# Optimization experiments

Hardware: AMD Instinct MI355X
Metric: run time of the kernel (lower is better)

The kernel has to match this reference:

```python
import jax, jax.numpy as jnp
import numpy as np

NUM_USERS = 100000
NUM_ITEMS = 50000
NUM_HIDDEN = 64
NUM_BINS = 10
BATCH = 131072
N_QUAD = 64  # quadrature nodes in incomplete/complete beta
EPS = 1e-6


def _trapz0(y, dt):
    # trapezoidal rule along axis 0 with uniform spacing dt
    return (jnp.sum(y, axis=0) - 0.5 * (y[0] + y[-1])) * dt


def setup_inputs() -> dict:
    key = jax.random.key(0)
    ks = jax.random.split(key, 12)
    return {
        "uid_input": jax.random.randint(ks[0], (BATCH,), 0, NUM_USERS),
        "iid_input": jax.random.randint(ks[1], (BATCH,), 0, NUM_ITEMS),
        "uid_features": 0.1 * jax.random.normal(ks[2], (NUM_USERS, NUM_HIDDEN + 1), jnp.float32),
        "iid_features": 0.1 * jax.random.normal(ks[3], (NUM_ITEMS, NUM_HIDDEN + 1), jnp.float32),
        "uid_bin_terms": 0.1 * jax.random.normal(ks[4], (NUM_USERS, NUM_BINS), jnp.float32),
        "iid_bin_terms": 0.1 * jax.random.normal(ks[5], (NUM_ITEMS, NUM_BINS), jnp.float32),
        "uid_alpha_emb": 0.01 * jax.random.normal(ks[6], (NUM_USERS, 1), jnp.float32),
        "uid_beta_emb": 0.01 * jax.random.normal(ks[7], (NUM_USERS, 1), jnp.float32),
        "iid_alpha_emb": 0.01 * jax.random.normal(ks[8], (NUM_ITEMS, 1), jnp.float32),
        "iid_beta_emb": 0.01 * jax.random.normal(ks[9], (NUM_ITEMS, 1), jnp.float32),
        "global_bias": jnp.asarray(2.0, jnp.float32),
    }


def reference(uid_input, iid_input, uid_features, iid_features,
              uid_bin_terms, iid_bin_terms, uid_alpha_emb, uid_beta_emb,
              iid_alpha_emb, iid_beta_emb, global_bias):
    # embedding lookups (confidence features alias the regular features)
    uf = uid_features[uid_input]          # (B, H+1)
    vf = iid_features[iid_input]          # (B, H+1)
    u = uf[:, :-1]                        # (B, H)
    v = vf[:, :-1]

    # mu / upsilon (upsilon_layer_id == 2: |dot|)
    dot = jnp.sum(u * v, axis=-1, keepdims=True)                    # (B, 1)
    len_prod = (jnp.linalg.norm(u, axis=1, keepdims=True)
                * jnp.linalg.norm(v, axis=1, keepdims=True))
    mu = jnp.clip(0.5 + 0.5 * dot / jnp.maximum(len_prod, EPS), EPS, 1.0 - EPS)
    upsilon = jnp.maximum(jnp.abs(dot), EPS)

    # alpha / beta
    alpha = jnp.maximum(0.01, mu * upsilon)
    beta = jnp.maximum(0.01, upsilon - alpha)
    alpha = global_bias + alpha
    beta = global_bias + beta
    alpha = jnp.maximum(0.01, alpha + uid_alpha_emb[uid_input] + iid_alpha_emb[iid_input])  # (B,1)
    beta = jnp.maximum(0.01, beta + uid_beta_emb[uid_input] + iid_beta_emb[iid_input])      # (B,1)

    # per-pair bin edges via normalized exp + cumsum
    terms = jnp.exp(uid_bin_terms[uid_input] + iid_bin_terms[iid_input])  # (B, NUM_BINS)
    terms = terms / jnp.sum(terms, axis=-1, keepdims=True)
    edges = jnp.cumsum(terms, axis=-1)                                    # (B, NUM_BINS)

    # regularized incomplete beta at interior edges via trapezoidal quadrature
    x = edges[:, :-1]                                  # (B, NB-1)
    t = jnp.linspace(0.0, 1.0, N_QUAD, dtype=alpha.dtype)
    dt = t[1] - t[0]
    t3 = t[:, None, None]                              # (n, 1, 1)
    a3 = alpha[None, :, :]                             # (1, B, 1)
    b3 = beta[None, :, :]
    tx = t3 * x[None]                                  # (n, B, NB-1)
    integrand = (tx ** (a3 - 1.0)) * ((1.0 - tx) ** (b3 - 1.0))
    integrand = integrand * (t3 <= x[None]).astype(integrand.dtype)
    Bx_ab = _trapz0(integrand, dt)                     # (B, NB-1)

    # complete beta B(a, b)
    c_int = (t[None, :] ** (alpha - 1.0)) * ((1.0 - t[None, :]) ** (beta - 1.0))  # (B, n)
    B_ab = (jnp.sum(c_int, axis=-1) - 0.5 * (c_int[:, 0] + c_int[:, -1])) * dt    # (B,)

    cdf = Bx_ab / B_ab[:, None]                        # (B, NB-1)
    cdf = jnp.concatenate([cdf, jnp.ones_like(alpha)], axis=-1)  # (B, NB)
    mass = jnp.concatenate([cdf[:, :1], cdf[:, 1:] - cdf[:, :-1]], axis=-1)
    return mass
```

## Files before the change

kernel.cpp:

```cpp
#include <hip/hip_runtime.h>
#include <math.h>

#define BLOCK 256

struct F4a4 { float a, b, c, d; };

__device__ __forceinline__ float exp2_fast(float x) {
#if __has_builtin(__builtin_amdgcn_exp2f)
    return __builtin_amdgcn_exp2f(x);
#else
    return __expf(x * 0.69314718055994531f);
#endif
}

__device__ __forceinline__ double exp_f64_fast(double x) {
    const double L2E = 1.4426950408889634074;
    const double LN2 = 0.69314718055994530942;
    double z = x * L2E;
    double n = rint(z);
    double r = fma(x, L2E, -n);
    double w = r * LN2;
    double p = 2.08767569878680989792e-9;
    p = fma(p, w, 2.50521083854417187751e-8);
    p = fma(p, w, 2.75573192239858906526e-7);
    p = fma(p, w, 2.75573192239858925110e-6);
    p = fma(p, w, 2.48015873015873015873e-5);
    p = fma(p, w, 1.98412698412698412698e-4);
    p = fma(p, w, 1.38888888888888888889e-3);
    p = fma(p, w, 8.33333333333333333333e-3);
    p = fma(p, w, 4.16666666666666666667e-2);
    p = fma(p, w, 1.66666666666666666667e-1);
    p = fma(p, w, 0.5);
    p = fma(p, w, 1.0);
    p = fma(p, w, 1.0);
    const int ni = (int)n;
    const double sc = __longlong_as_double((long long)(1023 + ni) << 52);
    return p * sc;
}

__global__ __launch_bounds__(BLOCK) void lbd_kernel(
    const int* __restrict__ uid_in, const int* __restrict__ iid_in,
    const float* __restrict__ uf,  const float* __restrict__ vf,
    const float* __restrict__ ubt, const float* __restrict__ ibt,
    const float* __restrict__ uae, const float* __restrict__ ube,
    const float* __restrict__ iae, const float* __restrict__ ibe,
    const float* __restrict__ gbp, float* __restrict__ out, int B)
{
    const int tid = threadIdx.x;
    const int sub = tid & 15;
    const int s0  = blockIdx.x * (BLOCK / 16) + (tid >> 4);
    const bool valid = (s0 < B);
    const int s = valid ? s0 : (B - 1);

    const int u = uid_in[s];
    const int v = iid_in[s];

    const F4a4 a = ((const F4a4*)(uf + (long long)u * 65))[sub];
    const F4a4 b = ((const F4a4*)(vf + (long long)v * 65))[sub];

    float dotp = a.a * b.a + a.b * b.b + a.c * b.c + a.d * b.d;
    float sup  = a.a * a.a + a.b * a.b + a.c * a.c + a.d * a.d;
    float svp  = b.a * b.a + b.b * b.b + b.c * b.c + b.d * b.d;
#pragma unroll
    for (int d = 1; d < 16; d <<= 1) {
        dotp += __shfl_xor(dotp, d, 64);
        sup  += __shfl_xor(sup,  d, 64);
        svp  += __shfl_xor(svp,  d, 64);
    }

    const float gb = gbp[0];
    const float len_prod = sqrtf(sup) * sqrtf(svp);
    const float EPS = 1e-6f;
    const float HI  = (float)(1.0 - 1e-6);
    float mu = 0.5f + (0.5f * dotp) / fmaxf(len_prod, EPS);
    mu = fminf(fmaxf(mu, EPS), HI);
    const float ups = fmaxf(fabsf(dotp), EPS);
    const float al0 = fmaxf(0.01f, mu * ups);
    const float be0 = fmaxf(0.01f, ups - al0);
    const float alpha = fmaxf(0.01f, (gb + al0) + uae[u] + iae[v]);
    const float beta  = fmaxf(0.01f, (gb + be0) + ube[u] + ibe[v]);
    const float am1 = alpha - 1.0f;
    const float bm1 = beta  - 1.0f;

    const double STEP = 1.0 / 63.0;
    float xf_own = 0.f, lx_own = 0.f;
    int   im_own = 0;
    {
        double e = 0.0;
        if (sub < 10)
            e = exp_f64_fast((double)ubt[u * 10 + sub] + (double)ibt[v * 10 + sub]);
        double c = e;
#pragma unroll
        for (int d = 1; d < 16; d <<= 1) {
            double t = __shfl_up(c, d, 16);
            if (sub >= d) c += t;
        }
        const double ssum = __shfl(c, 9, 16);
        if (sub < 9) {
            const double x = c / ssum;
            int k = (int)(x * 63.0);
            k = (k > 62) ? 62 : k;
            const int dec = ((double)k * STEP > x) ? 1 : 0;
            const int inc = ((k < 62) && ((double)(k + 1) * STEP <= x)) ? 1 : 0;
            im_own = k + inc - dec;
            xf_own = (float)x;
            lx_own = __log2f(xf_own);
        }
    }
    float xfj[9], alxj[9];
    int   imj[9];
#pragma unroll
    for (int j = 0; j < 9; ++j) {
        xfj[j]  = __shfl(xf_own, j, 16);
        alxj[j] = am1 * __shfl(lx_own, j, 16);
        imj[j]  = __shfl(im_own, j, 16);
    }

    float tfm[4], altm[4], l1m[4];
#pragma unroll
    for (int m = 0; m < 4; ++m) {
        const int i = m * 16 + sub;
        const float tf = (float)((double)i * STEP);
        tfm[m]  = tf;
        altm[m] = am1 * __log2f(tf);
        l1m[m]  = __log2f(1.0f - tf);
    }

    float accD = 0.0f;
    float acc[9];
#pragma unroll
    for (int j = 0; j < 9; ++j) acc[j] = 0.0f;

#pragma unroll
    for (int m = 0; m < 4; ++m)
        accD += exp2_fast(fmaf(bm1, l1m[m], altm[m]));

#pragma unroll
    for (int m = 0; m < 4; ++m) {
#pragma unroll
        for (int j = 0; j < 9; ++j) {
            const float w_ = fmaf(-tfm[m], xfj[j], 1.0f);
            const float e_ = fmaf(bm1, __log2f(w_), altm[m] + alxj[j]);
            const float y_ = exp2_fast(e_);
            const int   i_ = m * 16 + sub;
            acc[j] += ((unsigned)(i_ - 1) < (unsigned)imj[j]) ? y_ : 0.0f;
        }
    }

#pragma unroll
    for (int d = 1; d < 16; d <<= 1) {
        accD += __shfl_xor(accD, d, 64);
#pragma unroll
        for (int j = 0; j < 9; ++j) acc[j] += __shfl_xor(acc[j], d, 64);
    }

    const float dtf = (float)(1.0 / 63.0);
    const float Bab = accD * dtf;
    const float rB  = 1.0f / Bab;
    float cdfv[9];
#pragma unroll
    for (int j = 0; j < 9; ++j) cdfv[j] = (acc[j] * dtf) * rB;

    float mo = cdfv[0];
#pragma unroll
    for (int j = 1; j < 9; ++j) mo = (sub == j) ? (cdfv[j] - cdfv[j - 1]) : mo;
    mo = (sub == 9) ? (1.0f - cdfv[8]) : mo;
    if (valid && sub < 10) out[(long long)s * 10 + sub] = mo;
}

extern "C" void kernel_launch(void* const* d_in, const int* in_sizes, int n_in,
                              void* d_out, int out_size, void* d_ws, size_t ws_size,
                              hipStream_t stream) {
    (void)n_in; (void)out_size; (void)d_ws; (void)ws_size;
    const int*   uid = (const int*)d_in[0];
    const int*   iid = (const int*)d_in[1];
    const float* uf  = (const float*)d_in[2];
    const float* vf  = (const float*)d_in[3];
    const float* ubt = (const float*)d_in[4];
    const float* ibt = (const float*)d_in[5];
    const float* uae = (const float*)d_in[6];
    const float* ube = (const float*)d_in[7];
    const float* iae = (const float*)d_in[8];
    const float* ibe = (const float*)d_in[9];
    const float* gb  = (const float*)d_in[10];
    float* out = (float*)d_out;
    const int B = in_sizes[0];
    const int samples_per_block = BLOCK / 16;
    const int grid = (B + samples_per_block - 1) / samples_per_block;
    hipLaunchKernelGGL(lbd_kernel, dim3(grid), dim3(BLOCK), 0, stream,
                       uid, iid, uf, vf, ubt, ibt, uae, ube, iae, ibe, gb, out, B);
}
```

Baseline: 133.0 us.

## Use 4 lanes per sample with LDS node tables and wave-uniform early loop exit

Each sample now gets 4 lanes instead of 16, so every lane covers 16 quadrature nodes and 3 bin edges. The quadrature node values and their logs are precomputed once per block into shared memory. The per-edge integration loop now stops at a wave-uniform bound taken from the max edge index across the wave, which skips nodes past each edge that the mask would zero anyway. This reduces redundant log/exp work and the shuffle reduction depth, at the cost of more per-lane serial work, a __syncthreads, and a data-dependent loop trip count that may limit unrolling.

```diff
diff --git a/kernel.cpp b/kernel.cpp
--- a/kernel.cpp
+++ b/kernel.cpp
@@ -2,6 +2,7 @@
 #include <math.h>
 
 #define BLOCK 256
+#define SPB (BLOCK / 4)
 
 struct F4a4 { float a, b, c, d; };
 
@@ -16,8 +17,7 @@
 __device__ __forceinline__ double exp_f64_fast(double x) {
     const double L2E = 1.4426950408889634074;
     const double LN2 = 0.69314718055994530942;
-    double z = x * L2E;
-    double n = rint(z);
+    double n = rint(x * L2E);
     double r = fma(x, L2E, -n);
     double w = r * LN2;
     double p = 2.08767569878680989792e-9;
@@ -33,8 +33,7 @@
     p = fma(p, w, 0.5);
     p = fma(p, w, 1.0);
     p = fma(p, w, 1.0);
-    const int ni = (int)n;
-    const double sc = __longlong_as_double((long long)(1023 + ni) << 52);
+    const double sc = __longlong_as_double((long long)(1023 + (int)n) << 52);
     return p * sc;
 }
 
@@ -46,23 +45,41 @@
     const float* __restrict__ iae, const float* __restrict__ ibe,
     const float* __restrict__ gbp, float* __restrict__ out, int B)
 {
+    __shared__ float2 s_num[64];
+    __shared__ float2 s_den[64];
     const int tid = threadIdx.x;
-    const int sub = tid & 15;
-    const int s0  = blockIdx.x * (BLOCK / 16) + (tid >> 4);
+    if (tid < 64) {
+        const double STEP0 = 1.0 / 63.0;
+        float tf = (float)((double)tid * STEP0);
+        if (tid == 63) tf = 1.0f;
+        const float lt = __log2f(tf);
+        const float l1 = __log2f(1.0f - tf);
+        s_num[tid] = make_float2(tf, lt);
+        s_den[tid] = make_float2(lt, l1);
+    }
+    __syncthreads();
+
+    const int sub = tid & 3;
+    const int s0  = blockIdx.x * SPB + (tid >> 2);
     const bool valid = (s0 < B);
     const int s = valid ? s0 : (B - 1);
 
     const int u = uid_in[s];
     const int v = iid_in[s];
 
-    const F4a4 a = ((const F4a4*)(uf + (long long)u * 65))[sub];
-    const F4a4 b = ((const F4a4*)(vf + (long long)v * 65))[sub];
-
-    float dotp = a.a * b.a + a.b * b.b + a.c * b.c + a.d * b.d;
-    float sup  = a.a * a.a + a.b * a.b + a.c * a.c + a.d * a.d;
-    float svp  = b.a * b.a + b.b * b.b + b.c * b.c + b.d * b.d;
-#pragma unroll
-    for (int d = 1; d < 16; d <<= 1) {
+    const float* pu = uf + (long long)u * 65;
+    const float* pv = vf + (long long)v * 65;
+    float dotp = 0.f, sup = 0.f, svp = 0.f;
+#pragma unroll
+    for (int c = 0; c < 4; ++c) {
+        const F4a4 a = *(const F4a4*)(pu + c * 16 + sub * 4);
+        const F4a4 b = *(const F4a4*)(pv + c * 16 + sub * 4);
+        dotp += a.a * b.a + a.b * b.b + a.c * b.c + a.d * b.d;
+        sup  += a.a * a.a + a.b * a.b + a.c * a.c + a.d * a.d;
+        svp  += b.a * b.a + b.b * b.b + b.c * b.c + b.d * b.d;
+    }
+#pragma unroll
+    for (int d = 1; d < 4; d <<= 1) {
         dotp += __shfl_xor(dotp, d, 64);
         sup  += __shfl_xor(sup,  d, 64);
         svp  += __shfl_xor(svp,  d, 64);
@@ -83,89 +100,120 @@
     const float bm1 = beta  - 1.0f;
 
     const double STEP = 1.0 / 63.0;
-    float xf_own = 0.f, lx_own = 0.f;
-    int   im_own = 0;
+    const int lb = 3 * sub;
+    double e0, e1 = 0.0, e2 = 0.0;
     {
-        double e = 0.0;
-        if (sub < 10)
-            e = exp_f64_fast((double)ubt[u * 10 + sub] + (double)ibt[v * 10 + sub]);
-        double c = e;
-#pragma unroll
-        for (int d = 1; d < 16; d <<= 1) {
-            double t = __shfl_up(c, d, 16);
-            if (sub >= d) c += t;
-        }
-        const double ssum = __shfl(c, 9, 16);
-        if (sub < 9) {
-            const double x = c / ssum;
+        const long long ur = (long long)u * 10, vr = (long long)v * 10;
+        const int i1 = (lb + 1 <= 9) ? lb + 1 : 9;
+        const int i2 = (lb + 2 <= 9) ? lb + 2 : 9;
+        e0 = exp_f64_fast((double)ubt[ur + lb] + (double)ibt[vr + lb]);
+        const double t1 = exp_f64_fast((double)ubt[ur + i1] + (double)ibt[vr + i1]);
+        const double t2 = exp_f64_fast((double)ubt[ur + i2] + (double)ibt[vr + i2]);
+        if (lb + 1 <= 9) e1 = t1;
+        if (lb + 2 <= 9) e2 = t2;
+    }
+    const double c0 = e0, c1 = c0 + e1, c2 = c1 + e2;
+    double p = c2;
+#pragma unroll
+    for (int d = 1; d < 4; d <<= 1) {
+        const double t = __shfl_up(p, d, 4);
+        if (sub >= d) p += t;
+    }
+    const double ssum = __shfl(p, 3, 4);
+    const double ex   = p - c2;
+    float xf_own[3] = {0.f, 0.f, 0.f}, lx_own[3] = {0.f, 0.f, 0.f};
+    int   im_own[3] = {0, 0, 0};
+    const double cg0 = ex + c0, cg1 = ex + c1, cg2 = ex + c2;
+#pragma unroll
+    for (int r = 0; r < 3; ++r) {
+        const double cgr = (r == 0) ? cg0 : (r == 1) ? cg1 : cg2;
+        if (lb + r <= 8) {
+            const double x = cgr / ssum;
             int k = (int)(x * 63.0);
             k = (k > 62) ? 62 : k;
             const int dec = ((double)k * STEP > x) ? 1 : 0;
             const int inc = ((k < 62) && ((double)(k + 1) * STEP <= x)) ? 1 : 0;
-            im_own = k + inc - dec;
-            xf_own = (float)x;
-            lx_own = __log2f(xf_own);
+            im_own[r] = k + inc - dec;
+            xf_own[r] = (float)x;
+            lx_own[r] = __log2f(xf_own[r]);
         }
     }
+
     float xfj[9], alxj[9];
-    int   imj[9];
+    int   imj[9], Mw[9];
 #pragma unroll
     for (int j = 0; j < 9; ++j) {
-        xfj[j]  = __shfl(xf_own, j, 16);
-        alxj[j] = am1 * __shfl(lx_own, j, 16);
-        imj[j]  = __shfl(im_own, j, 16);
-    }
-
-    float tfm[4], altm[4], l1m[4];
-#pragma unroll
-    for (int m = 0; m < 4; ++m) {
-        const int i = m * 16 + sub;
-        const float tf = (float)((double)i * STEP);
-        tfm[m]  = tf;
-        altm[m] = am1 * __log2f(tf);
-        l1m[m]  = __log2f(1.0f - tf);
-    }
-
-    float accD = 0.0f;
+        const int src  = j / 3;
+        const int slot = j % 3;
+        const float xo = (slot == 0) ? xf_own[0] : (slot == 1) ? xf_own[1] : xf_own[2];
+        const float lo = (slot == 0) ? lx_own[0] : (slot == 1) ? lx_own[1] : lx_own[2];
+        const int   io = (slot == 0) ? im_own[0] : (slot == 1) ? im_own[1] : im_own[2];
+        xfj[j]  = __shfl(xo, src, 4);
+        alxj[j] = am1 * __shfl(lo, src, 4);
+        imj[j]  = __shfl(io, src, 4);
+        int mm = imj[j];
+        mm = max(mm, __shfl_xor(mm, 4, 64));
+        mm = max(mm, __shfl_xor(mm, 8, 64));
+        mm = max(mm, __shfl_xor(mm, 16, 64));
+        mm = max(mm, __shfl_xor(mm, 32, 64));
+        Mw[j] = __builtin_amdgcn_readfirstlane((mm >> 2) + 1);
+    }
+
+    float accD = 0.f;
+#pragma unroll
+    for (int m = 0; m < 16; ++m) {
+        const float2 dd = s_den[m * 4 + sub];
+        accD += exp2_fast(fmaf(bm1, dd.y, am1 * dd.x));
+    }
+
     float acc[9];
 #pragma unroll
-    for (int j = 0; j < 9; ++j) acc[j] = 0.0f;
-
-#pragma unroll
-    for (int m = 0; m < 4; ++m)
-        accD += exp2_fast(fmaf(bm1, l1m[m], altm[m]));
-
-#pragma unroll
-    for (int m = 0; m < 4; ++m) {
-#pragma unroll
-        for (int j = 0; j < 9; ++j) {
-            const float w_ = fmaf(-tfm[m], xfj[j], 1.0f);
-            const float e_ = fmaf(bm1, __log2f(w_), altm[m] + alxj[j]);
-            const float y_ = exp2_fast(e_);
-            const int   i_ = m * 16 + sub;
-            acc[j] += ((unsigned)(i_ - 1) < (unsigned)imj[j]) ? y_ : 0.0f;
+    for (int j = 0; j < 9; ++j) {
+        const float xj  = xfj[j];
+        const float axj = alxj[j];
+        const int   imv = imj[j];
+        const int   M   = Mw[j];
+        float a0 = 0.f;
+        for (int m = 0; m < M; ++m) {
+            const int i = m * 4 + sub;
+            const float2 tl = s_num[i];
+            const float w = fmaf(-tl.x, xj, 1.0f);
+            const float e = fmaf(bm1, __log2f(w), fmaf(am1, tl.y, axj));
+            const float y = exp2_fast(e);
+            a0 += ((unsigned)(i - 1) < (unsigned)imv) ? y : 0.f;
         }
-    }
-
-#pragma unroll
-    for (int d = 1; d < 16; d <<= 1) {
+        acc[j] = a0;
+    }
+
+#pragma unroll
+    for (int d = 1; d < 4; d <<= 1) {
         accD += __shfl_xor(accD, d, 64);
 #pragma unroll
         for (int j = 0; j < 9; ++j) acc[j] += __shfl_xor(acc[j], d, 64);
     }
 
     const float dtf = (float)(1.0 / 63.0);
-    const float Bab = accD * dtf;
-    const float rB  = 1.0f / Bab;
+    const float rB  = 1.0f / (accD * dtf);
     float cdfv[9];
 #pragma unroll
     for (int j = 0; j < 9; ++j) cdfv[j] = (acc[j] * dtf) * rB;
 
-    float mo = cdfv[0];
-#pragma unroll
-    for (int j = 1; j < 9; ++j) mo = (sub == j) ? (cdfv[j] - cdfv[j - 1]) : mo;
-    mo = (sub == 9) ? (1.0f - cdfv[8]) : mo;
-    if (valid && sub < 10) out[(long long)s * 10 + sub] = mo;
+    const float o0 = (sub == 0) ? cdfv[0]
+                   : (sub == 1) ? (cdfv[1] - cdfv[0])
+                   : (sub == 2) ? (cdfv[2] - cdfv[1])
+                   :              (cdfv[3] - cdfv[2]);
+    const float o1 = (sub == 0) ? (cdfv[4] - cdfv[3])
+                   : (sub == 1) ? (cdfv[5] - cdfv[4])
+                   : (sub == 2) ? (cdfv[6] - cdfv[5])
+                   :              (cdfv[7] - cdfv[6]);
+    const float o2 = (sub == 0) ? (cdfv[8] - cdfv[7])
+                   :              (1.0f - cdfv[8]);
+    if (valid) {
+        const long long ob = (long long)s * 10;
+        out[ob + sub]     = o0;
+        out[ob + 4 + sub] = o1;
+        if (sub < 2) out[ob + 8 + sub] = o2;
+    }
 }
 
 extern "C" void kernel_launch(void* const* d_in, const int* in_sizes, int n_in,
@@ -185,8 +233,7 @@
     const float* gb  = (const float*)d_in[10];
     float* out = (float*)d_out;
     const int B = in_sizes[0];
-    const int samples_per_block = BLOCK / 16;
-    const int grid = (B + samples_per_block - 1) / samples_per_block;
+    const int grid = (B + SPB - 1) / SPB;
     hipLaunchKernelGGL(lbd_kernel, dim3(grid), dim3(BLOCK), 0, stream,
                        uid, iid, uf, vf, ubt, ibt, uae, ube, iae, ibe, gb, out, B);
 }
```

Result: faster. 124.7 us (-6.2%).
